# Performance work log

Hardware: AMD Instinct MI355X
Metric: run time of the kernel (lower is better)

The kernel has to match this reference:

```python
import jax, jax.numpy as jnp
import numpy as np

B, S, DIM = 16, 8192, 128
H, KV, D = 4, 2, 64  # heads, kv_heads, dim_head


def setup_inputs() -> dict:
    key = jax.random.key(0)
    ks = jax.random.split(key, 8)
    scale = 0.05
    return {
        "x": jax.random.normal(ks[0], (B, S, DIM), dtype=jnp.float32),
        "Wq": jax.random.normal(ks[1], (H, D, DIM), dtype=jnp.float32) * scale,
        "bq": jax.random.normal(ks[2], (H, D), dtype=jnp.float32) * scale,
        "Wk": jax.random.normal(ks[3], (KV, D, DIM), dtype=jnp.float32) * scale,
        "bk": jax.random.normal(ks[4], (KV, D), dtype=jnp.float32) * scale,
        "Wv": jax.random.normal(ks[5], (KV, D, DIM), dtype=jnp.float32) * scale,
        "bv": jax.random.normal(ks[6], (KV, D), dtype=jnp.float32) * scale,
        "Wo": jax.random.normal(ks[7], (DIM, DIM), dtype=jnp.float32) * scale,
    }


def reference(x, Wq, bq, Wk, bk, Wv, bv, Wo):
    b, s, _ = x.shape
    # MultiHeadLinear: per-head Linear stacked on last axis -> [B,S,D,H]
    q_st = jnp.einsum("bsc,hdc->bsdh", x, Wq) + bq.T  # [B,S,D,H]
    k_st = jnp.einsum("bsc,hdc->bsdh", x, Wk) + bk.T  # [B,S,D,KV]
    v_st = jnp.einsum("bsc,hdc->bsdh", x, Wv) + bv.T  # [B,S,D,KV]
    # .view(B,-1,heads,dim_head): raw reshape of (D,H) block into (H,D)
    q = q_st.reshape(b, s, H, D)
    k = k_st.reshape(b, s, KV, D)
    v = v_st.reshape(b, s, KV, D)
    # k scaled by q mean over heads (no softmax anywhere)
    k = k * jnp.mean(q, axis=2, keepdims=True)  # [B,S,KV,D]
    attn = jnp.einsum("bshd,bskd->bshk", q, k) / jnp.sqrt(jnp.asarray(D, q.dtype))
    out = jnp.einsum("bshk,bskd->bshd", attn, v)  # [B,S,H,D]
    # reshape(B,-1,dim): [B,S,H*D=256] -> [B,2S,128]
    out = out.reshape(b, -1, DIM)
    return out @ Wo.T
```

## Files before the change

### kernel.cpp

```cpp
#include <hip/hip_runtime.h>
#include <stdint.h>


using short8 = __attribute__((ext_vector_type(8))) short;
using f32x4  = __attribute__((ext_vector_type(4))) float;

constexpr int XSTR = 136;
constexpr int PSTR = 10;
constexpr int T_TILES = 8;

__device__ __forceinline__ unsigned short f2bf(float f) {
    unsigned int u = __float_as_uint(f);
    u += 0x7FFFu + ((u >> 16) & 1u);
    return (unsigned short)(u >> 16);
}

__device__ __forceinline__ void barrier_nodrain() {
    asm volatile("s_waitcnt lgkmcnt(0)\n\ts_barrier" ::: "memory");
}

__global__ void prep_weights(const float* __restrict__ Wq, const float* __restrict__ bq,
                             const float* __restrict__ Wk, const float* __restrict__ bk,
                             const float* __restrict__ Wv, const float* __restrict__ bv,
                             const float* __restrict__ Wo,
                             unsigned short* __restrict__ Wp, float* __restrict__ bias)
{
    const int ch = blockIdx.x;
    const int c  = threadIdx.x;
    float w, b;
    if (ch < 256) {
        const int hh = ch & 3, dd = ch >> 2;
        w = Wq[(hh * 64 + dd) * 128 + c];
        b = bq[hh * 64 + dd];
    } else if (ch < 384) {
        const int i = ch - 256;
        const int kvh = i & 1, dd = i >> 1;
        w = Wk[(kvh * 64 + dd) * 128 + c];
        b = bk[kvh * 64 + dd];
    } else {
        const int i  = ch - 384;
        const int jg = i >> 6, kp = (i >> 4) & 3, jm = i & 15;
        const int j  = jg * 16 + jm;
        const int kv = kp >> 1, p = kp & 1;
        float acc = 0.f, bacc = 0.f;
        #pragma unroll 8
        for (int d = 0; d < 64; ++d) {
            const int idx = kv * 64 + d;
            const int kvh = idx & 1, dd = idx >> 1;
            const float wo = Wo[j * 128 + p * 64 + d];
            acc  += wo * Wv[(kvh * 64 + dd) * 128 + c];
            bacc += wo * bv[kvh * 64 + dd];
        }
        w = acc; b = bacc;
    }
    Wp[ch * 128 + c] = f2bf(w);
    if (c == 0) bias[ch] = b;
}

__device__ __forceinline__ void stage8_load(const float* __restrict__ x, int tb, int row0,
                                            int l, float4* xv)
{
    const int row = row0 + (l >> 3);
    const float* src = x + (size_t)(tb + row) * 128 + (l & 7) * 4;
    #pragma unroll
    for (int j = 0; j < 4; ++j) xv[j] = *(const float4*)(src + 32 * j);
}
__device__ __forceinline__ void stage8_write(unsigned short* __restrict__ xb, int row0,
                                             int l, const float4* xv)
{
    const int row = row0 + (l >> 3);
    #pragma unroll
    for (int j = 0; j < 4; ++j) {
        ushort4 s;
        s.x = f2bf(xv[j].x); s.y = f2bf(xv[j].y); s.z = f2bf(xv[j].z); s.w = f2bf(xv[j].w);
        *(ushort4*)&xb[row * XSTR + (l & 7) * 4 + 32 * j] = s;
    }
}

__global__ __launch_bounds__(768, 1)
void fused_attn_kernel(const float* __restrict__ x,
                       const unsigned short* __restrict__ Wp,
                       const float* __restrict__ bias,
                       float* __restrict__ out)
{
    __shared__ __align__(16) unsigned short xlds[3][64 * XSTR];
    __shared__ __align__(16) float partial[2][4][64][PSTR];
    __shared__ __align__(16) float coeff[64][8];

    const int tid = threadIdx.x;
    const int l   = tid & 63;
    const int wv  = tid >> 6;
    const int lr  = l & 15, lg = l >> 4;
    const int tok0 = blockIdx.x * (T_TILES * 64);

    if (wv < 4) {
        const int dc = wv;
        int chb[6];
        #pragma unroll
        for (int n = 0; n < 4; ++n) chb[n] = n * 64 + dc * 16;
        chb[4] = 256 + dc * 16;
        chb[5] = 320 + dc * 16;

        short8 areg[24];
        #pragma unroll
        for (int n = 0; n < 6; ++n)
            #pragma unroll
            for (int ks = 0; ks < 4; ++ks)
                areg[n * 4 + ks] = *(const short8*)(Wp + (size_t)(chb[n] + lr) * 128 + ks * 32 + lg * 8);
        f32x4 biasv[6];
        #pragma unroll
        for (int n = 0; n < 6; ++n)
            biasv[n] = *(const f32x4*)(bias + chb[n] + lg * 4);

        auto phase1 = [&](const unsigned short* __restrict__ xb, int pb) {
            #pragma unroll
            for (int p = 0; p < 4; ++p) {
                f32x4 acc[6];
                #pragma unroll
                for (int n = 0; n < 6; ++n) acc[n] = (f32x4){0.f, 0.f, 0.f, 0.f};
                #pragma unroll
                for (int ks = 0; ks < 4; ++ks) {
                    short8 bfr = *(const short8*)&xb[(p * 16 + lr) * XSTR + ks * 32 + lg * 8];
                    #pragma unroll
                    for (int n = 0; n < 6; ++n)
                        acc[n] = __builtin_amdgcn_mfma_f32_16x16x32_bf16(
                            areg[n * 4 + ks], bfr, acc[n], 0, 0, 0);
                }
                float pa[8];
                #pragma unroll
                for (int c = 0; c < 8; ++c) pa[c] = 0.f;
                #pragma unroll
                for (int r = 0; r < 4; ++r) {
                    const float q0 = acc[0][r] + biasv[0][r];
                    const float q1 = acc[1][r] + biasv[1][r];
                    const float q2 = acc[2][r] + biasv[2][r];
                    const float q3 = acc[3][r] + biasv[3][r];
                    const float k0v = acc[4][r] + biasv[4][r];
                    const float k1v = acc[5][r] + biasv[5][r];
                    const float qm  = 0.25f * (q0 + q1 + q2 + q3);
                    const float kt0 = k0v * qm, kt1 = k1v * qm;
                    pa[0] += q0 * kt0; pa[1] += q1 * kt0;
                    pa[2] += q0 * kt1; pa[3] += q1 * kt1;
                    pa[4] += q2 * kt0; pa[5] += q3 * kt0;
                    pa[6] += q2 * kt1; pa[7] += q3 * kt1;
                }
                #pragma unroll
                for (int c = 0; c < 8; ++c) pa[c] += __shfl_xor(pa[c], 16);
                #pragma unroll
                for (int c = 0; c < 8; ++c) pa[c] += __shfl_xor(pa[c], 32);
                if (lg == 0) {
                    float* dst = &partial[pb][dc][p * 16 + lr][0];
                    *(float2*)(dst)     = make_float2(pa[0], pa[1]);
                    *(float2*)(dst + 2) = make_float2(pa[2], pa[3]);
                    *(float2*)(dst + 4) = make_float2(pa[4], pa[5]);
                    *(float2*)(dst + 6) = make_float2(pa[6], pa[7]);
                }
            }
        };

        barrier_nodrain();
        phase1(xlds[0], 0);
        barrier_nodrain();

        for (int t = 0; t < T_TILES; ++t) {
            if (t < T_TILES - 1) phase1(xlds[(t + 1) % 3], (t + 1) & 1);
            barrier_nodrain();
        }
    } else {
        const int jg = wv - 4;

        short8 breg[16];
        #pragma unroll
        for (int kp = 0; kp < 4; ++kp)
            #pragma unroll
            for (int ks = 0; ks < 4; ++ks)
                breg[kp * 4 + ks] = *(const short8*)
                    (Wp + (size_t)(384 + jg * 64 + kp * 16 + lr) * 128 + ks * 32 + lg * 8);
        float bvv[4];
        #pragma unroll
        for (int kp = 0; kp < 4; ++kp)
            bvv[kp] = bias[384 + jg * 64 + kp * 16 + lr];

        {
            float4 xv[4];
            stage8_load(x, tok0, jg * 8, l, xv);
            stage8_write(xlds[0], jg * 8, l, xv);
        }
        barrier_nodrain();
        {
            float4 xv[4];
            stage8_load(x, tok0 + 64, jg * 8, l, xv);
            stage8_write(xlds[1], jg * 8, l, xv);
        }
        barrier_nodrain();

        for (int t = 0; t < T_TILES; ++t) {
            float4 xv[4];
            const bool do_stage = (t < T_TILES - 2);
            if (do_stage) stage8_load(x, tok0 + (t + 2) * 64, jg * 8, l, xv);

            {
                const int pb = t & 1;
                float s[8];
                #pragma unroll
                for (int c = 0; c < 8; ++c) s[c] = 0.f;
                #pragma unroll
                for (int dcc = 0; dcc < 4; ++dcc) {
                    const float* pr = &partial[pb][dcc][l][0];
                    #pragma unroll
                    for (int c = 0; c < 4; ++c) {
                        float2 v = *(const float2*)(pr + 2 * c);
                        s[2 * c] += v.x; s[2 * c + 1] += v.y;
                    }
                }
                float* cw = &coeff[l][0];
                *(float2*)(cw)     = make_float2(s[0] * 0.125f, s[1] * 0.125f);
                *(float2*)(cw + 2) = make_float2(s[2] * 0.125f, s[3] * 0.125f);
                *(float2*)(cw + 4) = make_float2(s[4] * 0.125f, s[5] * 0.125f);
                *(float2*)(cw + 6) = make_float2(s[6] * 0.125f, s[7] * 0.125f);
            }

            {
                const unsigned short* xb = xlds[t % 3];
                const int g0    = tok0 + t * 64;
                const int bb    = g0 >> 13;
                const int srow0 = bb * 16384 + 2 * (g0 & 8191);
                #pragma unroll
                for (int mf = 0; mf < 4; ++mf) {
                    f32x4 acc[4];
                    #pragma unroll
                    for (int kp = 0; kp < 4; ++kp) acc[kp] = (f32x4){0.f, 0.f, 0.f, 0.f};
                    #pragma unroll
                    for (int ks = 0; ks < 4; ++ks) {
                        short8 af = *(const short8*)&xb[(mf * 16 + lr) * XSTR + ks * 32 + lg * 8];
                        #pragma unroll
                        for (int kp = 0; kp < 4; ++kp)
                            acc[kp] = __builtin_amdgcn_mfma_f32_16x16x32_bf16(
                                af, breg[kp * 4 + ks], acc[kp], 0, 0, 0);
                    }
                    #pragma unroll
                    for (int r = 0; r < 4; ++r) {
                        const int tok = mf * 16 + lg * 4 + r;
                        f32x4 cl = *(const f32x4*)&coeff[tok][0];
                        f32x4 ch = *(const f32x4*)&coeff[tok][4];
                        const float a0 = acc[0][r] + bvv[0];
                        const float a1 = acc[1][r] + bvv[1];
                        const float a2 = acc[2][r] + bvv[2];
                        const float a3 = acc[3][r] + bvv[3];
                        const float o0 = cl[0] * a0 + cl[1] * a1 + cl[2] * a2 + cl[3] * a3;
                        const float o1 = ch[0] * a0 + ch[1] * a1 + ch[2] * a2 + ch[3] * a3;
                        const int row = srow0 + 32 * mf + 2 * (lg * 4 + r);
                        float* dst = out + (size_t)row * 128 + jg * 16 + lr;
                        __builtin_nontemporal_store(o0, dst);
                        __builtin_nontemporal_store(o1, dst + 128);
                    }
                }
            }

            if (do_stage) stage8_write(xlds[(t + 2) % 3], jg * 8, l, xv);
            barrier_nodrain();
        }
    }
}

extern "C" void kernel_launch(void* const* d_in, const int* in_sizes, int n_in,
                              void* d_out, int out_size, void* d_ws, size_t ws_size,
                              hipStream_t stream)
{
    (void)in_sizes; (void)n_in; (void)out_size; (void)ws_size;
    const float* x  = (const float*)d_in[0];
    const float* Wq = (const float*)d_in[1];
    const float* bq = (const float*)d_in[2];
    const float* Wk = (const float*)d_in[3];
    const float* bk = (const float*)d_in[4];
    const float* Wv = (const float*)d_in[5];
    const float* bv = (const float*)d_in[6];
    const float* Wo = (const float*)d_in[7];

    unsigned short* Wp   = (unsigned short*)d_ws;
    float*          bias = (float*)((char*)d_ws + 896 * 128 * 2);

    prep_weights<<<896, 128, 0, stream>>>(Wq, bq, Wk, bk, Wv, bv, Wo, Wp, bias);
    fused_attn_kernel<<<256, 768, 0, stream>>>(x, Wp, bias, (float*)d_out);
}
```

Baseline: 58.88 us.

## Split fused warp-specialized kernel into separate coefficient and V-projection kernels

The single warp-specialized kernel, in which four waves computed per-token attention coefficients and four waves did the V/Wo projection, is split into two kernels. The first writes the per-token coefficients to a global workspace, and the second reads them back together with x to produce the output. This gives more blocks and higher occupancy per kernel and removes the producer/consumer coupling. The cost is a second full read of x, an extra global round-trip for the coefficients, and an extra kernel launch.

```diff
diff --git a/kernel.cpp b/kernel.cpp
--- a/kernel.cpp
+++ b/kernel.cpp
@@ -7,7 +7,8 @@
 
 constexpr int XSTR = 136;
 constexpr int PSTR = 10;
-constexpr int T_TILES = 8;
+constexpr int TA = 4;
+constexpr int TB = 4;
 
 __device__ __forceinline__ unsigned short f2bf(float f) {
     unsigned int u = __float_as_uint(f);
@@ -77,189 +78,195 @@
     }
 }
 
-__global__ __launch_bounds__(768, 1)
-void fused_attn_kernel(const float* __restrict__ x,
-                       const unsigned short* __restrict__ Wp,
-                       const float* __restrict__ bias,
-                       float* __restrict__ out)
-{
-    __shared__ __align__(16) unsigned short xlds[3][64 * XSTR];
-    __shared__ __align__(16) float partial[2][4][64][PSTR];
-    __shared__ __align__(16) float coeff[64][8];
+__global__ __launch_bounds__(256, 2)
+void coeff_kernel(const float* __restrict__ x,
+                  const unsigned short* __restrict__ Wp,
+                  const float* __restrict__ bias,
+                  float* __restrict__ cg)
+{
+    __shared__ __align__(16) unsigned short xlds[64 * XSTR];
+    __shared__ __align__(16) float partial[4][64][PSTR];
 
     const int tid = threadIdx.x;
     const int l   = tid & 63;
     const int wv  = tid >> 6;
     const int lr  = l & 15, lg = l >> 4;
-    const int tok0 = blockIdx.x * (T_TILES * 64);
-
-    if (wv < 4) {
-        const int dc = wv;
-        int chb[6];
+    const int tok0 = blockIdx.x * (TA * 64);
+
+    const int dc = wv;
+    int chb[6];
+    #pragma unroll
+    for (int n = 0; n < 4; ++n) chb[n] = n * 64 + dc * 16;
+    chb[4] = 256 + dc * 16;
+    chb[5] = 320 + dc * 16;
+
+    short8 areg[24];
+    #pragma unroll
+    for (int n = 0; n < 6; ++n)
         #pragma unroll
-        for (int n = 0; n < 4; ++n) chb[n] = n * 64 + dc * 16;
-        chb[4] = 256 + dc * 16;
-        chb[5] = 320 + dc * 16;
-
-        short8 areg[24];
+        for (int ks = 0; ks < 4; ++ks)
+            areg[n * 4 + ks] = *(const short8*)(Wp + (size_t)(chb[n] + lr) * 128 + ks * 32 + lg * 8);
+    f32x4 biasv[6];
+    #pragma unroll
+    for (int n = 0; n < 6; ++n)
+        biasv[n] = *(const f32x4*)(bias + chb[n] + lg * 4);
+
+    float4 xa[4], xb_[4];
+    stage8_load(x, tok0, wv * 16,     l, xa);
+    stage8_load(x, tok0, wv * 16 + 8, l, xb_);
+
+    for (int t = 0; t < TA; ++t) {
+        stage8_write(xlds, wv * 16,     l, xa);
+        stage8_write(xlds, wv * 16 + 8, l, xb_);
+        if (t + 1 < TA) {
+            stage8_load(x, tok0 + (t + 1) * 64, wv * 16,     l, xa);
+            stage8_load(x, tok0 + (t + 1) * 64, wv * 16 + 8, l, xb_);
+        }
+        barrier_nodrain();
+
         #pragma unroll
-        for (int n = 0; n < 6; ++n)
-            #pragma unroll
-            for (int ks = 0; ks < 4; ++ks)
-                areg[n * 4 + ks] = *(const short8*)(Wp + (size_t)(chb[n] + lr) * 128 + ks * 32 + lg * 8);
-        f32x4 biasv[6];
+        for (int p = 0; p < 4; ++p) {
+            f32x4 acc[6];
+            #pragma unroll
+            for (int n = 0; n < 6; ++n) acc[n] = (f32x4){0.f, 0.f, 0.f, 0.f};
+            #pragma unroll
+            for (int ks = 0; ks < 4; ++ks) {
+                short8 bfr = *(const short8*)&xlds[(p * 16 + lr) * XSTR + ks * 32 + lg * 8];
+                #pragma unroll
+                for (int n = 0; n < 6; ++n)
+                    acc[n] = __builtin_amdgcn_mfma_f32_16x16x32_bf16(
+                        areg[n * 4 + ks], bfr, acc[n], 0, 0, 0);
+            }
+            float pa[8];
+            #pragma unroll
+            for (int c = 0; c < 8; ++c) pa[c] = 0.f;
+            #pragma unroll
+            for (int r = 0; r < 4; ++r) {
+                const float q0 = acc[0][r] + biasv[0][r];
+                const float q1 = acc[1][r] + biasv[1][r];
+                const float q2 = acc[2][r] + biasv[2][r];
+                const float q3 = acc[3][r] + biasv[3][r];
+                const float k0v = acc[4][r] + biasv[4][r];
+                const float k1v = acc[5][r] + biasv[5][r];
+                const float qm  = 0.25f * (q0 + q1 + q2 + q3);
+                const float kt0 = k0v * qm, kt1 = k1v * qm;
+                pa[0] += q0 * kt0; pa[1] += q1 * kt0;
+                pa[2] += q0 * kt1; pa[3] += q1 * kt1;
+                pa[4] += q2 * kt0; pa[5] += q3 * kt0;
+                pa[6] += q2 * kt1; pa[7] += q3 * kt1;
+            }
+            #pragma unroll
+            for (int c = 0; c < 8; ++c) pa[c] += __shfl_xor(pa[c], 16);
+            #pragma unroll
+            for (int c = 0; c < 8; ++c) pa[c] += __shfl_xor(pa[c], 32);
+            if (lg == 0) {
+                float* dst = &partial[dc][p * 16 + lr][0];
+                *(float2*)(dst)     = make_float2(pa[0], pa[1]);
+                *(float2*)(dst + 2) = make_float2(pa[2], pa[3]);
+                *(float2*)(dst + 4) = make_float2(pa[4], pa[5]);
+                *(float2*)(dst + 6) = make_float2(pa[6], pa[7]);
+            }
+        }
+        barrier_nodrain();
+
+        {
+            const int tok = tid >> 2;
+            const int c2  = (tid & 3) * 2;
+            float s0 = 0.f, s1 = 0.f;
+            #pragma unroll
+            for (int dcc = 0; dcc < 4; ++dcc) {
+                float2 v = *(const float2*)&partial[dcc][tok][c2];
+                s0 += v.x; s1 += v.y;
+            }
+            *(float2*)&cg[(size_t)(tok0 + t * 64 + tok) * 8 + c2] =
+                make_float2(s0 * 0.125f, s1 * 0.125f);
+        }
+        barrier_nodrain();
+    }
+}
+
+__global__ __launch_bounds__(512, 4)
+void vproj_kernel(const float* __restrict__ x,
+                  const unsigned short* __restrict__ Wp,
+                  const float* __restrict__ bias,
+                  const float* __restrict__ cg,
+                  float* __restrict__ out)
+{
+    __shared__ __align__(16) unsigned short xlds[64 * XSTR];
+    __shared__ __align__(16) float clds[64][8];
+
+    const int tid = threadIdx.x;
+    const int l   = tid & 63;
+    const int wv  = tid >> 6;
+    const int lr  = l & 15, lg = l >> 4;
+    const int jg  = wv;
+    const int tok0 = blockIdx.x * (TB * 64);
+
+    short8 breg[16];
+    #pragma unroll
+    for (int kp = 0; kp < 4; ++kp)
         #pragma unroll
-        for (int n = 0; n < 6; ++n)
-            biasv[n] = *(const f32x4*)(bias + chb[n] + lg * 4);
-
-        auto phase1 = [&](const unsigned short* __restrict__ xb, int pb) {
-            #pragma unroll
-            for (int p = 0; p < 4; ++p) {
-                f32x4 acc[6];
-                #pragma unroll
-                for (int n = 0; n < 6; ++n) acc[n] = (f32x4){0.f, 0.f, 0.f, 0.f};
+        for (int ks = 0; ks < 4; ++ks)
+            breg[kp * 4 + ks] = *(const short8*)
+                (Wp + (size_t)(384 + jg * 64 + kp * 16 + lr) * 128 + ks * 32 + lg * 8);
+    float bvv[4];
+    #pragma unroll
+    for (int kp = 0; kp < 4; ++kp)
+        bvv[kp] = bias[384 + jg * 64 + kp * 16 + lr];
+
+    float4 xv[4];
+    float2 cv = make_float2(0.f, 0.f);
+    stage8_load(x, tok0, wv * 8, l, xv);
+    if (tid < 256)
+        cv = *(const float2*)&cg[(size_t)(tok0 + (tid >> 2)) * 8 + (tid & 3) * 2];
+
+    for (int t = 0; t < TB; ++t) {
+        stage8_write(xlds, wv * 8, l, xv);
+        if (tid < 256)
+            *(float2*)&clds[tid >> 2][(tid & 3) * 2] = cv;
+        if (t + 1 < TB) {
+            stage8_load(x, tok0 + (t + 1) * 64, wv * 8, l, xv);
+            if (tid < 256)
+                cv = *(const float2*)&cg[(size_t)(tok0 + (t + 1) * 64 + (tid >> 2)) * 8 + (tid & 3) * 2];
+        }
+        barrier_nodrain();
+
+        {
+            const int g0    = tok0 + t * 64;
+            const int bb    = g0 >> 13;
+            const int srow0 = bb * 16384 + 2 * (g0 & 8191);
+            #pragma unroll
+            for (int mf = 0; mf < 4; ++mf) {
+                f32x4 acc[4];
+                #pragma unroll
+                for (int kp = 0; kp < 4; ++kp) acc[kp] = (f32x4){0.f, 0.f, 0.f, 0.f};
                 #pragma unroll
                 for (int ks = 0; ks < 4; ++ks) {
-                    short8 bfr = *(const short8*)&xb[(p * 16 + lr) * XSTR + ks * 32 + lg * 8];
+                    short8 af = *(const short8*)&xlds[(mf * 16 + lr) * XSTR + ks * 32 + lg * 8];
                     #pragma unroll
-                    for (int n = 0; n < 6; ++n)
-                        acc[n] = __builtin_amdgcn_mfma_f32_16x16x32_bf16(
-                            areg[n * 4 + ks], bfr, acc[n], 0, 0, 0);
+                    for (int kp = 0; kp < 4; ++kp)
+                        acc[kp] = __builtin_amdgcn_mfma_f32_16x16x32_bf16(
+                            af, breg[kp * 4 + ks], acc[kp], 0, 0, 0);
                 }
-                float pa[8];
-                #pragma unroll
-                for (int c = 0; c < 8; ++c) pa[c] = 0.f;
                 #pragma unroll
                 for (int r = 0; r < 4; ++r) {
-                    const float q0 = acc[0][r] + biasv[0][r];
-                    const float q1 = acc[1][r] + biasv[1][r];
-                    const float q2 = acc[2][r] + biasv[2][r];
-                    const float q3 = acc[3][r] + biasv[3][r];
-                    const float k0v = acc[4][r] + biasv[4][r];
-                    const float k1v = acc[5][r] + biasv[5][r];
-                    const float qm  = 0.25f * (q0 + q1 + q2 + q3);
-                    const float kt0 = k0v * qm, kt1 = k1v * qm;
-                    pa[0] += q0 * kt0; pa[1] += q1 * kt0;
-                    pa[2] += q0 * kt1; pa[3] += q1 * kt1;
-                    pa[4] += q2 * kt0; pa[5] += q3 * kt0;
-                    pa[6] += q2 * kt1; pa[7] += q3 * kt1;
+                    const int tok = mf * 16 + lg * 4 + r;
+                    f32x4 cl = *(const f32x4*)&clds[tok][0];
+                    f32x4 ch = *(const f32x4*)&clds[tok][4];
+                    const float a0 = acc[0][r] + bvv[0];
+                    const float a1 = acc[1][r] + bvv[1];
+                    const float a2 = acc[2][r] + bvv[2];
+                    const float a3 = acc[3][r] + bvv[3];
+                    const float o0 = cl[0] * a0 + cl[1] * a1 + cl[2] * a2 + cl[3] * a3;
+                    const float o1 = ch[0] * a0 + ch[1] * a1 + ch[2] * a2 + ch[3] * a3;
+                    const int row = srow0 + 32 * mf + 2 * (lg * 4 + r);
+                    float* dst = out + (size_t)row * 128 + jg * 16 + lr;
+                    __builtin_nontemporal_store(o0, dst);
+                    __builtin_nontemporal_store(o1, dst + 128);
                 }
-                #pragma unroll
-                for (int c = 0; c < 8; ++c) pa[c] += __shfl_xor(pa[c], 16);
-                #pragma unroll
-                for (int c = 0; c < 8; ++c) pa[c] += __shfl_xor(pa[c], 32);
-                if (lg == 0) {
-                    float* dst = &partial[pb][dc][p * 16 + lr][0];
-                    *(float2*)(dst)     = make_float2(pa[0], pa[1]);
-                    *(float2*)(dst + 2) = make_float2(pa[2], pa[3]);
-                    *(float2*)(dst + 4) = make_float2(pa[4], pa[5]);
-                    *(float2*)(dst + 6) = make_float2(pa[6], pa[7]);
-                }
-            }
-        };
-
-        barrier_nodrain();
-        phase1(xlds[0], 0);
-        barrier_nodrain();
-
-        for (int t = 0; t < T_TILES; ++t) {
-            if (t < T_TILES - 1) phase1(xlds[(t + 1) % 3], (t + 1) & 1);
-            barrier_nodrain();
-        }
-    } else {
-        const int jg = wv - 4;
-
-        short8 breg[16];
-        #pragma unroll
-        for (int kp = 0; kp < 4; ++kp)
-            #pragma unroll
-            for (int ks = 0; ks < 4; ++ks)
-                breg[kp * 4 + ks] = *(const short8*)
-                    (Wp + (size_t)(384 + jg * 64 + kp * 16 + lr) * 128 + ks * 32 + lg * 8);
-        float bvv[4];
-        #pragma unroll
-        for (int kp = 0; kp < 4; ++kp)
-            bvv[kp] = bias[384 + jg * 64 + kp * 16 + lr];
-
-        {
-            float4 xv[4];
-            stage8_load(x, tok0, jg * 8, l, xv);
-            stage8_write(xlds[0], jg * 8, l, xv);
-        }
-        barrier_nodrain();
-        {
-            float4 xv[4];
-            stage8_load(x, tok0 + 64, jg * 8, l, xv);
-            stage8_write(xlds[1], jg * 8, l, xv);
-        }
-        barrier_nodrain();
-
-        for (int t = 0; t < T_TILES; ++t) {
-            float4 xv[4];
-            const bool do_stage = (t < T_TILES - 2);
-            if (do_stage) stage8_load(x, tok0 + (t + 2) * 64, jg * 8, l, xv);
-
-            {
-                const int pb = t & 1;
-                float s[8];
-                #pragma unroll
-                for (int c = 0; c < 8; ++c) s[c] = 0.f;
-                #pragma unroll
-                for (int dcc = 0; dcc < 4; ++dcc) {
-                    const float* pr = &partial[pb][dcc][l][0];
-                    #pragma unroll
-                    for (int c = 0; c < 4; ++c) {
-                        float2 v = *(const float2*)(pr + 2 * c);
-                        s[2 * c] += v.x; s[2 * c + 1] += v.y;
-                    }
-                }
-                float* cw = &coeff[l][0];
-                *(float2*)(cw)     = make_float2(s[0] * 0.125f, s[1] * 0.125f);
-                *(float2*)(cw + 2) = make_float2(s[2] * 0.125f, s[3] * 0.125f);
-                *(float2*)(cw + 4) = make_float2(s[4] * 0.125f, s[5] * 0.125f);
-                *(float2*)(cw + 6) = make_float2(s[6] * 0.125f, s[7] * 0.125f);
-            }
-
-            {
-                const unsigned short* xb = xlds[t % 3];
-                const int g0    = tok0 + t * 64;
-                const int bb    = g0 >> 13;
-                const int srow0 = bb * 16384 + 2 * (g0 & 8191);
-                #pragma unroll
-                for (int mf = 0; mf < 4; ++mf) {
-                    f32x4 acc[4];
-                    #pragma unroll
-                    for (int kp = 0; kp < 4; ++kp) acc[kp] = (f32x4){0.f, 0.f, 0.f, 0.f};
-                    #pragma unroll
-                    for (int ks = 0; ks < 4; ++ks) {
-                        short8 af = *(const short8*)&xb[(mf * 16 + lr) * XSTR + ks * 32 + lg * 8];
-                        #pragma unroll
-                        for (int kp = 0; kp < 4; ++kp)
-                            acc[kp] = __builtin_amdgcn_mfma_f32_16x16x32_bf16(
-                                af, breg[kp * 4 + ks], acc[kp], 0, 0, 0);
-                    }
-                    #pragma unroll
-                    for (int r = 0; r < 4; ++r) {
-                        const int tok = mf * 16 + lg * 4 + r;
-                        f32x4 cl = *(const f32x4*)&coeff[tok][0];
-                        f32x4 ch = *(const f32x4*)&coeff[tok][4];
-                        const float a0 = acc[0][r] + bvv[0];
-                        const float a1 = acc[1][r] + bvv[1];
-                        const float a2 = acc[2][r] + bvv[2];
-                        const float a3 = acc[3][r] + bvv[3];
-                        const float o0 = cl[0] * a0 + cl[1] * a1 + cl[2] * a2 + cl[3] * a3;
-                        const float o1 = ch[0] * a0 + ch[1] * a1 + ch[2] * a2 + ch[3] * a3;
-                        const int row = srow0 + 32 * mf + 2 * (lg * 4 + r);
-                        float* dst = out + (size_t)row * 128 + jg * 16 + lr;
-                        __builtin_nontemporal_store(o0, dst);
-                        __builtin_nontemporal_store(o1, dst + 128);
-                    }
-                }
-            }
-
-            if (do_stage) stage8_write(xlds[(t + 2) % 3], jg * 8, l, xv);
-            barrier_nodrain();
-        }
+            }
+        }
+        barrier_nodrain();
     }
 }
 
@@ -279,7 +286,9 @@
 
     unsigned short* Wp   = (unsigned short*)d_ws;
     float*          bias = (float*)((char*)d_ws + 896 * 128 * 2);
+    float*          cg   = (float*)((char*)d_ws + 896 * 128 * 2 + 4096);
 
     prep_weights<<<896, 128, 0, stream>>>(Wq, bq, Wk, bk, Wv, bv, Wo, Wp, bias);
-    fused_attn_kernel<<<256, 768, 0, stream>>>(x, Wp, bias, (float*)d_out);
-}
+    coeff_kernel<<<512, 256, 0, stream>>>(x, Wp, bias, cg);
+    vproj_kernel<<<512, 512, 0, stream>>>(x, Wp, bias, cg, (float*)d_out);
+}
```

New measurement: 88.77 us. 1.51x slower.

## Shrink block to 512 threads with two output column groups per wave

Applied to the files above, without the earlier changes.

Cuts the block from 12 waves to 8 (launch bounds 512 threads, 2 blocks per CU). Each epilogue wave now covers two output column groups, with the Wo-fused weights permuted so that each lane writes float2 pairs. The x staging is split across all 8 waves and reads use nontemporal loads. Per-wave coefficient buffers replace the shared one, and s_setprio is raised around the MFMA loops. The aim is to cut per-CU wave overhead and let two blocks overlap, at the cost of more registers per epilogue wave and a changed pipeline ordering.

```diff
diff --git a/kernel.cpp b/kernel.cpp
--- a/kernel.cpp
+++ b/kernel.cpp
@@ -4,6 +4,7 @@
 
 using short8 = __attribute__((ext_vector_type(8))) short;
 using f32x4  = __attribute__((ext_vector_type(4))) float;
+using f32x2  = __attribute__((ext_vector_type(2))) float;
 
 constexpr int XSTR = 136;
 constexpr int PSTR = 10;
@@ -40,7 +41,7 @@
     } else {
         const int i  = ch - 384;
         const int jg = i >> 6, kp = (i >> 4) & 3, jm = i & 15;
-        const int j  = jg * 16 + jm;
+        const int j  = (jg >> 1) * 32 + jm * 2 + (jg & 1);
         const int kv = kp >> 1, p = kp & 1;
         float acc = 0.f, bacc = 0.f;
         #pragma unroll 8
@@ -58,26 +59,26 @@
 }
 
 __device__ __forceinline__ void stage8_load(const float* __restrict__ x, int tb, int row0,
-                                            int l, float4* xv)
+                                            int l, f32x4* xv)
 {
     const int row = row0 + (l >> 3);
-    const float* src = x + (size_t)(tb + row) * 128 + (l & 7) * 4;
+    const f32x4* src = (const f32x4*)(x + (size_t)(tb + row) * 128) + (l & 7);
     #pragma unroll
-    for (int j = 0; j < 4; ++j) xv[j] = *(const float4*)(src + 32 * j);
+    for (int j = 0; j < 4; ++j) xv[j] = __builtin_nontemporal_load(src + 8 * j);
 }
 __device__ __forceinline__ void stage8_write(unsigned short* __restrict__ xb, int row0,
-                                             int l, const float4* xv)
+                                             int l, const f32x4* xv)
 {
     const int row = row0 + (l >> 3);
     #pragma unroll
     for (int j = 0; j < 4; ++j) {
         ushort4 s;
-        s.x = f2bf(xv[j].x); s.y = f2bf(xv[j].y); s.z = f2bf(xv[j].z); s.w = f2bf(xv[j].w);
+        s.x = f2bf(xv[j][0]); s.y = f2bf(xv[j][1]); s.z = f2bf(xv[j][2]); s.w = f2bf(xv[j][3]);
         *(ushort4*)&xb[row * XSTR + (l & 7) * 4 + 32 * j] = s;
     }
 }
 
-__global__ __launch_bounds__(768, 1)
+__global__ __launch_bounds__(512, 2)
 void fused_attn_kernel(const float* __restrict__ x,
                        const unsigned short* __restrict__ Wp,
                        const float* __restrict__ bias,
@@ -85,7 +86,7 @@
 {
     __shared__ __align__(16) unsigned short xlds[3][64 * XSTR];
     __shared__ __align__(16) float partial[2][4][64][PSTR];
-    __shared__ __align__(16) float coeff[64][8];
+    __shared__ __align__(16) float coeffw[4][64][8];
 
     const int tid = threadIdx.x;
     const int l   = tid & 63;
@@ -95,6 +96,7 @@
 
     if (wv < 4) {
         const int dc = wv;
+        const int row0 = dc * 8;
         int chb[6];
         #pragma unroll
         for (int n = 0; n < 4; ++n) chb[n] = n * 64 + dc * 16;
@@ -118,6 +120,7 @@
                 f32x4 acc[6];
                 #pragma unroll
                 for (int n = 0; n < 6; ++n) acc[n] = (f32x4){0.f, 0.f, 0.f, 0.f};
+                __builtin_amdgcn_s_setprio(1);
                 #pragma unroll
                 for (int ks = 0; ks < 4; ++ks) {
                     short8 bfr = *(const short8*)&xb[(p * 16 + lr) * XSTR + ks * 32 + lg * 8];
@@ -126,6 +129,7 @@
                         acc[n] = __builtin_amdgcn_mfma_f32_16x16x32_bf16(
                             areg[n * 4 + ks], bfr, acc[n], 0, 0, 0);
                 }
+                __builtin_amdgcn_s_setprio(0);
                 float pa[8];
                 #pragma unroll
                 for (int c = 0; c < 8; ++c) pa[c] = 0.f;
@@ -158,46 +162,52 @@
             }
         };
 
+        f32x4 xv[4];
+        stage8_load(x, tok0, row0, l, xv);
+        stage8_write(xlds[0], row0, l, xv);
+        stage8_load(x, tok0 + 64, row0, l, xv);
         barrier_nodrain();
         phase1(xlds[0], 0);
-        barrier_nodrain();
 
         for (int t = 0; t < T_TILES; ++t) {
-            if (t < T_TILES - 1) phase1(xlds[(t + 1) % 3], (t + 1) & 1);
+            stage8_write(xlds[(t + 1) % 3], row0, l, xv);
+            const int tl = (t + 2 < T_TILES) ? t + 2 : T_TILES - 1;
+            stage8_load(x, tok0 + tl * 64, row0, l, xv);
             barrier_nodrain();
+            if (t + 1 < T_TILES)
+                phase1(xlds[(t + 1) % 3], (t + 1) & 1);
         }
     } else {
-        const int jg = wv - 4;
-
-        short8 breg[16];
-        #pragma unroll
-        for (int kp = 0; kp < 4; ++kp)
+        const int jgp  = wv - 4;
+        const int row0 = 32 + jgp * 8;
+
+        short8 breg[32];
+        #pragma unroll
+        for (int j2 = 0; j2 < 2; ++j2)
             #pragma unroll
-            for (int ks = 0; ks < 4; ++ks)
-                breg[kp * 4 + ks] = *(const short8*)
-                    (Wp + (size_t)(384 + jg * 64 + kp * 16 + lr) * 128 + ks * 32 + lg * 8);
-        float bvv[4];
-        #pragma unroll
-        for (int kp = 0; kp < 4; ++kp)
-            bvv[kp] = bias[384 + jg * 64 + kp * 16 + lr];
-
-        {
-            float4 xv[4];
-            stage8_load(x, tok0, jg * 8, l, xv);
-            stage8_write(xlds[0], jg * 8, l, xv);
-        }
+            for (int kp = 0; kp < 4; ++kp)
+                #pragma unroll
+                for (int ks = 0; ks < 4; ++ks)
+                    breg[(j2 * 4 + kp) * 4 + ks] = *(const short8*)
+                        (Wp + (size_t)(384 + (jgp * 2 + j2) * 64 + kp * 16 + lr) * 128 + ks * 32 + lg * 8);
+        float bvv[2][4];
+        #pragma unroll
+        for (int j2 = 0; j2 < 2; ++j2)
+            #pragma unroll
+            for (int kp = 0; kp < 4; ++kp)
+                bvv[j2][kp] = bias[384 + (jgp * 2 + j2) * 64 + kp * 16 + lr];
+
+        f32x4 xv[4];
+        stage8_load(x, tok0, row0, l, xv);
+        stage8_write(xlds[0], row0, l, xv);
+        stage8_load(x, tok0 + 64, row0, l, xv);
         barrier_nodrain();
-        {
-            float4 xv[4];
-            stage8_load(x, tok0 + 64, jg * 8, l, xv);
-            stage8_write(xlds[1], jg * 8, l, xv);
-        }
-        barrier_nodrain();
 
         for (int t = 0; t < T_TILES; ++t) {
-            float4 xv[4];
-            const bool do_stage = (t < T_TILES - 2);
-            if (do_stage) stage8_load(x, tok0 + (t + 2) * 64, jg * 8, l, xv);
+            stage8_write(xlds[(t + 1) % 3], row0, l, xv);
+            const int tl = (t + 2 < T_TILES) ? t + 2 : T_TILES - 1;
+            stage8_load(x, tok0 + tl * 64, row0, l, xv);
+            barrier_nodrain();
 
             {
                 const int pb = t & 1;
@@ -213,7 +223,7 @@
                         s[2 * c] += v.x; s[2 * c + 1] += v.y;
                     }
                 }
-                float* cw = &coeff[l][0];
+                float* cw = &coeffw[jgp][l][0];
                 *(float2*)(cw)     = make_float2(s[0] * 0.125f, s[1] * 0.125f);
                 *(float2*)(cw + 2) = make_float2(s[2] * 0.125f, s[3] * 0.125f);
                 *(float2*)(cw + 4) = make_float2(s[4] * 0.125f, s[5] * 0.125f);
@@ -227,38 +237,54 @@
                 const int srow0 = bb * 16384 + 2 * (g0 & 8191);
                 #pragma unroll
                 for (int mf = 0; mf < 4; ++mf) {
-                    f32x4 acc[4];
-                    #pragma unroll
-                    for (int kp = 0; kp < 4; ++kp) acc[kp] = (f32x4){0.f, 0.f, 0.f, 0.f};
+                    f32x4 a2[2][4];
+                    #pragma unroll
+                    for (int j2 = 0; j2 < 2; ++j2)
+                        #pragma unroll
+                        for (int kp = 0; kp < 4; ++kp)
+                            a2[j2][kp] = (f32x4){0.f, 0.f, 0.f, 0.f};
+                    __builtin_amdgcn_s_setprio(1);
                     #pragma unroll
                     for (int ks = 0; ks < 4; ++ks) {
                         short8 af = *(const short8*)&xb[(mf * 16 + lr) * XSTR + ks * 32 + lg * 8];
                         #pragma unroll
-                        for (int kp = 0; kp < 4; ++kp)
-                            acc[kp] = __builtin_amdgcn_mfma_f32_16x16x32_bf16(
-                                af, breg[kp * 4 + ks], acc[kp], 0, 0, 0);
+                        for (int j2 = 0; j2 < 2; ++j2)
+                            #pragma unroll
+                            for (int kp = 0; kp < 4; ++kp)
+                                a2[j2][kp] = __builtin_amdgcn_mfma_f32_16x16x32_bf16(
+                                    af, breg[(j2 * 4 + kp) * 4 + ks], a2[j2][kp], 0, 0, 0);
                     }
+                    __builtin_amdgcn_s_setprio(0);
                     #pragma unroll
                     for (int r = 0; r < 4; ++r) {
-                        const int tok = mf * 16 + lg * 4 + r;
-                        f32x4 cl = *(const f32x4*)&coeff[tok][0];
-                        f32x4 ch = *(const f32x4*)&coeff[tok][4];
-                        const float a0 = acc[0][r] + bvv[0];
-                        const float a1 = acc[1][r] + bvv[1];
-                        const float a2 = acc[2][r] + bvv[2];
-                        const float a3 = acc[3][r] + bvv[3];
-                        const float o0 = cl[0] * a0 + cl[1] * a1 + cl[2] * a2 + cl[3] * a3;
-                        const float o1 = ch[0] * a0 + ch[1] * a1 + ch[2] * a2 + ch[3] * a3;
-                        const int row = srow0 + 32 * mf + 2 * (lg * 4 + r);
-                        float* dst = out + (size_t)row * 128 + jg * 16 + lr;
-                        __builtin_nontemporal_store(o0, dst);
-                        __builtin_nontemporal_store(o1, dst + 128);
+                        const int tokL = lg * 4 + r;
+                        const int tok  = mf * 16 + tokL;
+                        f32x4 cl = *(const f32x4*)&coeffw[jgp][tok][0];
+                        f32x4 ch = *(const f32x4*)&coeffw[jgp][tok][4];
+                        f32x2 s0, s1;
+                        {
+                            const float a0 = a2[0][0][r] + bvv[0][0];
+                            const float a1 = a2[0][1][r] + bvv[0][1];
+                            const float av = a2[0][2][r] + bvv[0][2];
+                            const float a3 = a2[0][3][r] + bvv[0][3];
+                            s0[0] = cl[0] * a0 + cl[1] * a1 + cl[2] * av + cl[3] * a3;
+                            s1[0] = ch[0] * a0 + ch[1] * a1 + ch[2] * av + ch[3] * a3;
+                        }
+                        {
+                            const float a0 = a2[1][0][r] + bvv[1][0];
+                            const float a1 = a2[1][1][r] + bvv[1][1];
+                            const float av = a2[1][2][r] + bvv[1][2];
+                            const float a3 = a2[1][3][r] + bvv[1][3];
+                            s0[1] = cl[0] * a0 + cl[1] * a1 + cl[2] * av + cl[3] * a3;
+                            s1[1] = ch[0] * a0 + ch[1] * a1 + ch[2] * av + ch[3] * a3;
+                        }
+                        const int row = srow0 + 32 * mf + 2 * tokL;
+                        float* dst = out + (size_t)row * 128 + jgp * 32 + lr * 2;
+                        __builtin_nontemporal_store(s0, (f32x2*)(dst));
+                        __builtin_nontemporal_store(s1, (f32x2*)(dst + 128));
                     }
                 }
             }
-
-            if (do_stage) stage8_write(xlds[(t + 2) % 3], jg * 8, l, xv);
-            barrier_nodrain();
         }
     }
 }
@@ -281,5 +307,5 @@
     float*          bias = (float*)((char*)d_ws + 896 * 128 * 2);
 
     prep_weights<<<896, 128, 0, stream>>>(Wq, bq, Wk, bk, Wv, bv, Wo, Wp, bias);
-    fused_attn_kernel<<<256, 768, 0, stream>>>(x, Wp, bias, (float*)d_out);
-}
+    fused_attn_kernel<<<256, 512, 0, stream>>>(x, Wp, bias, (float*)d_out);
+}
```

Result: slower. 61.36 us (+4.2%).

## Replace warp-specialized producer/consumer split with uniform 8-wave blocks

Applied to the files above, without the earlier changes.

Removes the warp specialization, in which 4 waves did the Q/K projection and 4 waves did the V/out projection. Now all 8 waves of a 512-thread block do both stages: each wave handles half the token rows of the Q/K phase for one d-chunk, plus its own 16-column slice of the V/out phase. Launch bounds change to 512 threads with 2 blocks per CU, aiming for more resident waves and for every wave to load global data and issue MFMAs. The cost is higher register pressure, since each wave now holds both the areg and breg weight fragments, which may cause spills under the tighter bound. It also keeps a per-wave copy of the coefficient buffer in shared memory.

```diff
diff --git a/kernel.cpp b/kernel.cpp
--- a/kernel.cpp
+++ b/kernel.cpp
@@ -77,7 +77,7 @@
     }
 }
 
-__global__ __launch_bounds__(768, 1)
+__global__ __launch_bounds__(512, 2)
 void fused_attn_kernel(const float* __restrict__ x,
                        const unsigned short* __restrict__ Wp,
                        const float* __restrict__ bias,
@@ -85,7 +85,7 @@
 {
     __shared__ __align__(16) unsigned short xlds[3][64 * XSTR];
     __shared__ __align__(16) float partial[2][4][64][PSTR];
-    __shared__ __align__(16) float coeff[64][8];
+    __shared__ __align__(16) float coeffw[8][64][8];
 
     const int tid = threadIdx.x;
     const int l   = tid & 63;
@@ -93,173 +93,166 @@
     const int lr  = l & 15, lg = l >> 4;
     const int tok0 = blockIdx.x * (T_TILES * 64);
 
-    if (wv < 4) {
-        const int dc = wv;
-        int chb[6];
+    const int dc = wv & 3;
+    const int th = wv >> 2;
+    int chb[6];
+    #pragma unroll
+    for (int n = 0; n < 4; ++n) chb[n] = n * 64 + dc * 16;
+    chb[4] = 256 + dc * 16;
+    chb[5] = 320 + dc * 16;
+
+    short8 areg[24];
+    #pragma unroll
+    for (int n = 0; n < 6; ++n)
         #pragma unroll
-        for (int n = 0; n < 4; ++n) chb[n] = n * 64 + dc * 16;
-        chb[4] = 256 + dc * 16;
-        chb[5] = 320 + dc * 16;
-
-        short8 areg[24];
+        for (int ks = 0; ks < 4; ++ks)
+            areg[n * 4 + ks] = *(const short8*)(Wp + (size_t)(chb[n] + lr) * 128 + ks * 32 + lg * 8);
+    f32x4 biasv[6];
+    #pragma unroll
+    for (int n = 0; n < 6; ++n)
+        biasv[n] = *(const f32x4*)(bias + chb[n] + lg * 4);
+
+    const int jg = wv;
+    short8 breg[16];
+    #pragma unroll
+    for (int kp = 0; kp < 4; ++kp)
         #pragma unroll
-        for (int n = 0; n < 6; ++n)
-            #pragma unroll
-            for (int ks = 0; ks < 4; ++ks)
-                areg[n * 4 + ks] = *(const short8*)(Wp + (size_t)(chb[n] + lr) * 128 + ks * 32 + lg * 8);
-        f32x4 biasv[6];
+        for (int ks = 0; ks < 4; ++ks)
+            breg[kp * 4 + ks] = *(const short8*)
+                (Wp + (size_t)(384 + jg * 64 + kp * 16 + lr) * 128 + ks * 32 + lg * 8);
+    float bvv[4];
+    #pragma unroll
+    for (int kp = 0; kp < 4; ++kp)
+        bvv[kp] = bias[384 + jg * 64 + kp * 16 + lr];
+
+    auto phase1 = [&](const unsigned short* __restrict__ xb, int pb) {
         #pragma unroll
-        for (int n = 0; n < 6; ++n)
-            biasv[n] = *(const f32x4*)(bias + chb[n] + lg * 4);
-
-        auto phase1 = [&](const unsigned short* __restrict__ xb, int pb) {
-            #pragma unroll
-            for (int p = 0; p < 4; ++p) {
-                f32x4 acc[6];
-                #pragma unroll
-                for (int n = 0; n < 6; ++n) acc[n] = (f32x4){0.f, 0.f, 0.f, 0.f};
+        for (int p = 0; p < 2; ++p) {
+            const int trow = th * 32 + p * 16;
+            f32x4 acc[6];
+            #pragma unroll
+            for (int n = 0; n < 6; ++n) acc[n] = (f32x4){0.f, 0.f, 0.f, 0.f};
+            #pragma unroll
+            for (int ks = 0; ks < 4; ++ks) {
+                short8 bfr = *(const short8*)&xb[(trow + lr) * XSTR + ks * 32 + lg * 8];
+                #pragma unroll
+                for (int n = 0; n < 6; ++n)
+                    acc[n] = __builtin_amdgcn_mfma_f32_16x16x32_bf16(
+                        areg[n * 4 + ks], bfr, acc[n], 0, 0, 0);
+            }
+            float pa[8];
+            #pragma unroll
+            for (int c = 0; c < 8; ++c) pa[c] = 0.f;
+            #pragma unroll
+            for (int r = 0; r < 4; ++r) {
+                const float q0 = acc[0][r] + biasv[0][r];
+                const float q1 = acc[1][r] + biasv[1][r];
+                const float q2 = acc[2][r] + biasv[2][r];
+                const float q3 = acc[3][r] + biasv[3][r];
+                const float k0v = acc[4][r] + biasv[4][r];
+                const float k1v = acc[5][r] + biasv[5][r];
+                const float qm  = 0.25f * (q0 + q1 + q2 + q3);
+                const float kt0 = k0v * qm, kt1 = k1v * qm;
+                pa[0] += q0 * kt0; pa[1] += q1 * kt0;
+                pa[2] += q0 * kt1; pa[3] += q1 * kt1;
+                pa[4] += q2 * kt0; pa[5] += q3 * kt0;
+                pa[6] += q2 * kt1; pa[7] += q3 * kt1;
+            }
+            #pragma unroll
+            for (int c = 0; c < 8; ++c) pa[c] += __shfl_xor(pa[c], 16);
+            #pragma unroll
+            for (int c = 0; c < 8; ++c) pa[c] += __shfl_xor(pa[c], 32);
+            if (lg == 0) {
+                float* dst = &partial[pb][dc][trow + lr][0];
+                *(float2*)(dst)     = make_float2(pa[0], pa[1]);
+                *(float2*)(dst + 2) = make_float2(pa[2], pa[3]);
+                *(float2*)(dst + 4) = make_float2(pa[4], pa[5]);
+                *(float2*)(dst + 6) = make_float2(pa[6], pa[7]);
+            }
+        }
+    };
+
+    auto finalize_phase2 = [&](const unsigned short* __restrict__ xb, int t) {
+        {
+            const int pb = t & 1;
+            float s[8];
+            #pragma unroll
+            for (int c = 0; c < 8; ++c) s[c] = 0.f;
+            #pragma unroll
+            for (int dcc = 0; dcc < 4; ++dcc) {
+                const float* pr = &partial[pb][dcc][l][0];
+                #pragma unroll
+                for (int c = 0; c < 4; ++c) {
+                    float2 v = *(const float2*)(pr + 2 * c);
+                    s[2 * c] += v.x; s[2 * c + 1] += v.y;
+                }
+            }
+            float* cw = &coeffw[wv][l][0];
+            *(float2*)(cw)     = make_float2(s[0] * 0.125f, s[1] * 0.125f);
+            *(float2*)(cw + 2) = make_float2(s[2] * 0.125f, s[3] * 0.125f);
+            *(float2*)(cw + 4) = make_float2(s[4] * 0.125f, s[5] * 0.125f);
+            *(float2*)(cw + 6) = make_float2(s[6] * 0.125f, s[7] * 0.125f);
+        }
+        {
+            const int g0    = tok0 + t * 64;
+            const int bb    = g0 >> 13;
+            const int srow0 = bb * 16384 + 2 * (g0 & 8191);
+            #pragma unroll
+            for (int mf = 0; mf < 4; ++mf) {
+                f32x4 acc[4];
+                #pragma unroll
+                for (int kp = 0; kp < 4; ++kp) acc[kp] = (f32x4){0.f, 0.f, 0.f, 0.f};
                 #pragma unroll
                 for (int ks = 0; ks < 4; ++ks) {
-                    short8 bfr = *(const short8*)&xb[(p * 16 + lr) * XSTR + ks * 32 + lg * 8];
+                    short8 af = *(const short8*)&xb[(mf * 16 + lr) * XSTR + ks * 32 + lg * 8];
                     #pragma unroll
-                    for (int n = 0; n < 6; ++n)
-                        acc[n] = __builtin_amdgcn_mfma_f32_16x16x32_bf16(
-                            areg[n * 4 + ks], bfr, acc[n], 0, 0, 0);
+                    for (int kp = 0; kp < 4; ++kp)
+                        acc[kp] = __builtin_amdgcn_mfma_f32_16x16x32_bf16(
+                            af, breg[kp * 4 + ks], acc[kp], 0, 0, 0);
                 }
-                float pa[8];
-                #pragma unroll
-                for (int c = 0; c < 8; ++c) pa[c] = 0.f;
                 #pragma unroll
                 for (int r = 0; r < 4; ++r) {
-                    const float q0 = acc[0][r] + biasv[0][r];
-                    const float q1 = acc[1][r] + biasv[1][r];
-                    const float q2 = acc[2][r] + biasv[2][r];
-                    const float q3 = acc[3][r] + biasv[3][r];
-                    const float k0v = acc[4][r] + biasv[4][r];
-                    const float k1v = acc[5][r] + biasv[5][r];
-                    const float qm  = 0.25f * (q0 + q1 + q2 + q3);
-                    const float kt0 = k0v * qm, kt1 = k1v * qm;
-                    pa[0] += q0 * kt0; pa[1] += q1 * kt0;
-                    pa[2] += q0 * kt1; pa[3] += q1 * kt1;
-                    pa[4] += q2 * kt0; pa[5] += q3 * kt0;
-                    pa[6] += q2 * kt1; pa[7] += q3 * kt1;
+                    const int tokL = lg * 4 + r;
+                    const int tok  = mf * 16 + tokL;
+                    f32x4 cl = *(const f32x4*)&coeffw[wv][tok][0];
+                    f32x4 ch = *(const f32x4*)&coeffw[wv][tok][4];
+                    const float a0 = acc[0][r] + bvv[0];
+                    const float a1 = acc[1][r] + bvv[1];
+                    const float a2 = acc[2][r] + bvv[2];
+                    const float a3 = acc[3][r] + bvv[3];
+                    const float o0 = cl[0] * a0 + cl[1] * a1 + cl[2] * a2 + cl[3] * a3;
+                    const float o1 = ch[0] * a0 + ch[1] * a1 + ch[2] * a2 + ch[3] * a3;
+                    const int row = srow0 + 32 * mf + 2 * tokL;
+                    float* dst = out + (size_t)row * 128 + jg * 16 + lr;
+                    __builtin_nontemporal_store(o0, dst);
+                    __builtin_nontemporal_store(o1, dst + 128);
                 }
-                #pragma unroll
-                for (int c = 0; c < 8; ++c) pa[c] += __shfl_xor(pa[c], 16);
-                #pragma unroll
-                for (int c = 0; c < 8; ++c) pa[c] += __shfl_xor(pa[c], 32);
-                if (lg == 0) {
-                    float* dst = &partial[pb][dc][p * 16 + lr][0];
-                    *(float2*)(dst)     = make_float2(pa[0], pa[1]);
-                    *(float2*)(dst + 2) = make_float2(pa[2], pa[3]);
-                    *(float2*)(dst + 4) = make_float2(pa[4], pa[5]);
-                    *(float2*)(dst + 6) = make_float2(pa[6], pa[7]);
-                }
-            }
-        };
-
+            }
+        }
+    };
+
+    {
+        float4 xv[4];
+        stage8_load(x, tok0, wv * 8, l, xv);
+        stage8_write(xlds[0], wv * 8, l, xv);
+    }
+    barrier_nodrain();
+    {
+        float4 xv[4];
+        stage8_load(x, tok0 + 64, wv * 8, l, xv);
+        phase1(xlds[0], 0);
+        stage8_write(xlds[1], wv * 8, l, xv);
+    }
+    barrier_nodrain();
+
+    for (int t = 0; t < T_TILES; ++t) {
+        float4 xv[4];
+        const bool do_stage = (t < T_TILES - 2);
+        if (do_stage) stage8_load(x, tok0 + (t + 2) * 64, wv * 8, l, xv);
+        finalize_phase2(xlds[t % 3], t);
+        if (t < T_TILES - 1) phase1(xlds[(t + 1) % 3], (t + 1) & 1);
+        if (do_stage) stage8_write(xlds[(t + 2) % 3], wv * 8, l, xv);
         barrier_nodrain();
-        phase1(xlds[0], 0);
-        barrier_nodrain();
-
-        for (int t = 0; t < T_TILES; ++t) {
-            if (t < T_TILES - 1) phase1(xlds[(t + 1) % 3], (t + 1) & 1);
-            barrier_nodrain();
-        }
-    } else {
-        const int jg = wv - 4;
-
-        short8 breg[16];
-        #pragma unroll
-        for (int kp = 0; kp < 4; ++kp)
-            #pragma unroll
-            for (int ks = 0; ks < 4; ++ks)
-                breg[kp * 4 + ks] = *(const short8*)
-                    (Wp + (size_t)(384 + jg * 64 + kp * 16 + lr) * 128 + ks * 32 + lg * 8);
-        float bvv[4];
-        #pragma unroll
-        for (int kp = 0; kp < 4; ++kp)
-            bvv[kp] = bias[384 + jg * 64 + kp * 16 + lr];
-
-        {
-            float4 xv[4];
-            stage8_load(x, tok0, jg * 8, l, xv);
-            stage8_write(xlds[0], jg * 8, l, xv);
-        }
-        barrier_nodrain();
-        {
-            float4 xv[4];
-            stage8_load(x, tok0 + 64, jg * 8, l, xv);
-            stage8_write(xlds[1], jg * 8, l, xv);
-        }
-        barrier_nodrain();
-
-        for (int t = 0; t < T_TILES; ++t) {
-            float4 xv[4];
-            const bool do_stage = (t < T_TILES - 2);
-            if (do_stage) stage8_load(x, tok0 + (t + 2) * 64, jg * 8, l, xv);
-
-            {
-                const int pb = t & 1;
-                float s[8];
-                #pragma unroll
-                for (int c = 0; c < 8; ++c) s[c] = 0.f;
-                #pragma unroll
-                for (int dcc = 0; dcc < 4; ++dcc) {
-                    const float* pr = &partial[pb][dcc][l][0];
-                    #pragma unroll
-                    for (int c = 0; c < 4; ++c) {
-                        float2 v = *(const float2*)(pr + 2 * c);
-                        s[2 * c] += v.x; s[2 * c + 1] += v.y;
-                    }
-                }
-                float* cw = &coeff[l][0];
-                *(float2*)(cw)     = make_float2(s[0] * 0.125f, s[1] * 0.125f);
-                *(float2*)(cw + 2) = make_float2(s[2] * 0.125f, s[3] * 0.125f);
-                *(float2*)(cw + 4) = make_float2(s[4] * 0.125f, s[5] * 0.125f);
-                *(float2*)(cw + 6) = make_float2(s[6] * 0.125f, s[7] * 0.125f);
-            }
-
-            {
-                const unsigned short* xb = xlds[t % 3];
-                const int g0    = tok0 + t * 64;
-                const int bb    = g0 >> 13;
-                const int srow0 = bb * 16384 + 2 * (g0 & 8191);
-                #pragma unroll
-                for (int mf = 0; mf < 4; ++mf) {
-                    f32x4 acc[4];
-                    #pragma unroll
-                    for (int kp = 0; kp < 4; ++kp) acc[kp] = (f32x4){0.f, 0.f, 0.f, 0.f};
-                    #pragma unroll
-                    for (int ks = 0; ks < 4; ++ks) {
-                        short8 af = *(const short8*)&xb[(mf * 16 + lr) * XSTR + ks * 32 + lg * 8];
-                        #pragma unroll
-                        for (int kp = 0; kp < 4; ++kp)
-                            acc[kp] = __builtin_amdgcn_mfma_f32_16x16x32_bf16(
-                                af, breg[kp * 4 + ks], acc[kp], 0, 0, 0);
-                    }
-                    #pragma unroll
-                    for (int r = 0; r < 4; ++r) {
-                        const int tok = mf * 16 + lg * 4 + r;
-                        f32x4 cl = *(const f32x4*)&coeff[tok][0];
-                        f32x4 ch = *(const f32x4*)&coeff[tok][4];
-                        const float a0 = acc[0][r] + bvv[0];
-                        const float a1 = acc[1][r] + bvv[1];
-                        const float a2 = acc[2][r] + bvv[2];
-                        const float a3 = acc[3][r] + bvv[3];
-                        const float o0 = cl[0] * a0 + cl[1] * a1 + cl[2] * a2 + cl[3] * a3;
-                        const float o1 = ch[0] * a0 + ch[1] * a1 + ch[2] * a2 + ch[3] * a3;
-                        const int row = srow0 + 32 * mf + 2 * (lg * 4 + r);
-                        float* dst = out + (size_t)row * 128 + jg * 16 + lr;
-                        __builtin_nontemporal_store(o0, dst);
-                        __builtin_nontemporal_store(o1, dst + 128);
-                    }
-                }
-            }
-
-            if (do_stage) stage8_write(xlds[(t + 2) % 3], jg * 8, l, xv);
-            barrier_nodrain();
-        }
     }
 }
 
@@ -281,5 +274,5 @@
     float*          bias = (float*)((char*)d_ws + 896 * 128 * 2);
 
     prep_weights<<<896, 128, 0, stream>>>(Wq, bq, Wk, bk, Wv, bv, Wo, Wp, bias);
-    fused_attn_kernel<<<256, 768, 0, stream>>>(x, Wp, bias, (float*)d_out);
-}
+    fused_attn_kernel<<<256, 512, 0, stream>>>(x, Wp, bias, (float*)d_out);
+}
```

After: 65.44 us. +11.1%, slower.
